# Kernel optimization log

Hardware: AMD Instinct MI355X
Metric: run time of the kernel (lower is better)

## Reference

```python
import jax, jax.numpy as jnp
import numpy as np

B, N = 16, 1023            # batch, signal length
T = N + 1                  # frames: hop=1, gaussian centers 0..N
F_BINS = N + 1             # rfft(2N) -> N+1 frequency bins
HID, NCLS = 128, 10


def setup_inputs() -> dict:
    key = jax.random.key(0)
    k = jax.random.split(key, 3)
    x = jax.random.normal(k[0], (B, N), dtype=jnp.float32)
    lambd = jnp.asarray(32.0, dtype=jnp.float32)  # learnable window width (sigma)
    feat = F_BINS * T
    W1 = jax.random.normal(k[1], (HID, feat), dtype=jnp.float32) / np.float32(np.sqrt(feat))
    b1 = jnp.zeros((HID,), jnp.float32)
    W2 = jax.random.normal(k[2], (NCLS, HID), dtype=jnp.float32) / np.float32(np.sqrt(HID))
    b2 = jnp.zeros((NCLS,), jnp.float32)
    return {"x": x, "lambd": lambd, "W1": W1, "b1": b1, "W2": W2, "b2": b2}


def _spectrogram(x, lambd):
    """Whole-signal differentiable Gaussian spectrogram (non-optimized path, hop=1).

    S[b, f, t] = | sum_n (x[b,n]-mean) * exp(-0.5*((n-t)/|lambd|)^2) * e^{-2pi i f n / (2N)} |^2
    Vectorized over the batch (replaces the per-sample Python loop).
    """
    n = x.shape[-1]
    sigma = jnp.abs(lambd)
    t = jnp.arange(n, dtype=jnp.float32)
    tc = jnp.arange(n + 1, dtype=jnp.float32)  # frame centers 0..n (n//hop + 1 frames)
    win = jnp.exp(-0.5 * ((t[None, :] - tc[:, None]) / sigma) ** 2)  # [T, n]
    xc = x - jnp.mean(x, axis=-1, keepdims=True)                     # per-sample mean removal
    xw = xc[:, None, :] * win[None]                                  # [B, T, n]
    spec = jnp.abs(jnp.fft.rfft(xw, n=2 * n, axis=-1)) ** 2          # [B, T, n+1]
    return jnp.transpose(spec, (0, 2, 1))[:, None]                   # [B, 1, n+1, T]


def reference(x, lambd, W1, b1, W2, b2):
    s = _spectrogram(x, lambd)                       # [B, 1, F_BINS, T]
    flat = s.reshape(s.shape[0], -1)                 # [B, F_BINS*T]
    h = jax.nn.relu(flat @ W1.T + b1)                # fc1 + relu
    out = h @ W2.T + b2                              # fc2
    return out, s
```

## Files before the change

### kernel.cpp

```cpp
#include <hip/hip_runtime.h>
#include <math.h>

#define NSIG   1023
#define BATCH  16
#define FT     1024
#define KW     256
#define RHALF  128
#define XPAD   1280
#define HID    128

#define OFF_XCP  0u
#define OFF_G    20480u
#define OFF_HRAW 20736u
#define OFF_TAB  22784u
#define TAB_ECH  0u
#define TAB_ECL  262144u
#define TAB_ESH  524288u
#define TAB_ESL  786432u

typedef int    i32x4  __attribute__((ext_vector_type(4)));
typedef float  f32x4  __attribute__((ext_vector_type(4)));
typedef __bf16 bf16x8 __attribute__((ext_vector_type(8)));
typedef unsigned short u16;

static __device__ __forceinline__ unsigned bfbits(float v) {
    unsigned u = __builtin_bit_cast(unsigned, v);
    return (u + 0x7fffu + ((u >> 16) & 1u)) >> 16;
}

__global__ void k_prep(const float* __restrict__ x, float* __restrict__ ws) {
    int b = blockIdx.x;
    __shared__ float red[256];
    float s = 0.f;
    for (int i = threadIdx.x; i < NSIG; i += 256) s += x[b * NSIG + i];
    red[threadIdx.x] = s;
    __syncthreads();
    for (int o = 128; o > 0; o >>= 1) {
        if (threadIdx.x < o) red[threadIdx.x] += red[threadIdx.x + o];
        __syncthreads();
    }
    float mean = red[0] * (1.0f / NSIG);
    float* xcp = ws + OFF_XCP + b * XPAD;
    for (int i = threadIdx.x; i < XPAD; i += 256) {
        int n = i - RHALF;
        xcp[i] = (n >= 0 && n < NSIG) ? (x[b * NSIG + n] - mean) : 0.f;
    }
}

__global__ void k_tables(const float* __restrict__ lambd, float* __restrict__ ws) {
    int bid = blockIdx.x;
    if (bid == 1024) {
        float sigma = fabsf(lambd[0]);
        float inv2s2 = 0.5f / (sigma * sigma);
        for (int i = threadIdx.x; i < KW; i += 256) {
            float d = (float)(i - RHALF);
            ws[OFF_G + i] = expf(-d * d * inv2s2);
        }
        for (int i = threadIdx.x; i < 2048; i += 256) ws[OFF_HRAW + i] = 0.f;
        return;
    }
    int idx = bid * 256 + threadIdx.x;
    int f = idx >> 8, k = idx & 255;
    int d = k - RHALF;
    int p = f * d;
    int m = p % 2046; if (m < 0) m += 2046;
    double ang = (double)m * (6.283185307179586476925286766559 / 2046.0);
    double sv, cv;
    sincos(ang, &sv, &cv);
    float cf = (float)cv, sf = (float)sv;
    u16* tab = (u16*)(ws + OFF_TAB);
    unsigned chb = bfbits(cf);
    float chf = __builtin_bit_cast(float, chb << 16);
    unsigned clb = bfbits(cf - chf);
    unsigned shb = bfbits(sf);
    float shf = __builtin_bit_cast(float, shb << 16);
    unsigned slb = bfbits(sf - shf);
    tab[TAB_ECH + idx] = (u16)chb;
    tab[TAB_ECL + idx] = (u16)clb;
    tab[TAB_ESH + idx] = (u16)shb;
    tab[TAB_ESL + idx] = (u16)slb;
}

__global__ __launch_bounds__(512, 4) void k_spec(const float* __restrict__ ws,
                                                 float* __restrict__ out) {
    __shared__ u16 yH[64 * 256];
    __shared__ u16 yL[64 * 256];
    int t0 = blockIdx.x * 64, f0 = blockIdx.y * 128, b = blockIdx.z;
    int tid = threadIdx.x;
    int wave = tid >> 6, lane = tid & 63;
    int lo = lane & 15, hi4 = lane >> 4;
    const u16* tab = (const u16*)(ws + OFF_TAB);
    const float* xcp = ws + OFF_XCP + b * XPAD;
    const float* gw  = ws + OFF_G;

    #pragma unroll
    for (int i = 0; i < 4; i++) {
        int idx = tid + i * 512;
        int t = idx >> 5, kg = idx & 31;
        int k = kg * 8;
        const float* xp = xcp + t0 + t + k;
        float4 g0 = *(const float4*)&gw[k];
        float4 g1 = *(const float4*)&gw[k + 4];
        float yv[8];
        yv[0] = xp[0] * g0.x; yv[1] = xp[1] * g0.y;
        yv[2] = xp[2] * g0.z; yv[3] = xp[3] * g0.w;
        yv[4] = xp[4] * g1.x; yv[5] = xp[5] * g1.y;
        yv[6] = xp[6] * g1.z; yv[7] = xp[7] * g1.w;
        unsigned hb[8], lb[8];
        #pragma unroll
        for (int j = 0; j < 8; j++) {
            unsigned u = __builtin_bit_cast(unsigned, yv[j]);
            unsigned h = (u + 0x7fffu + ((u >> 16) & 1u)) & 0xffff0000u;
            float hf = __builtin_bit_cast(float, h);
            hb[j] = h >> 16;
            lb[j] = bfbits(yv[j] - hf);
        }
        i32x4 ph, pl;
        ph.x = (int)(hb[0] | (hb[1] << 16)); ph.y = (int)(hb[2] | (hb[3] << 16));
        ph.z = (int)(hb[4] | (hb[5] << 16)); ph.w = (int)(hb[6] | (hb[7] << 16));
        pl.x = (int)(lb[0] | (lb[1] << 16)); pl.y = (int)(lb[2] | (lb[3] << 16));
        pl.z = (int)(lb[4] | (lb[5] << 16)); pl.w = (int)(lb[6] | (lb[7] << 16));
        int wb = ((t * 512 + kg * 16) ^ ((t & 7) << 4));
        *(i32x4*)((char*)yH + wb) = ph;
        *(i32x4*)((char*)yL + wb) = pl;
    }
    __syncthreads();

    size_t arow = (size_t)(f0 + wave * 16 + lo) * 256 + hi4 * 8;
    const u16* pech = tab + TAB_ECH + arow;
    const u16* pecl = tab + TAB_ECL + arow;
    const u16* pesh = tab + TAB_ESH + arow;
    const u16* pesl = tab + TAB_ESL + arow;

    f32x4 reA[4], imA[4];
    #pragma unroll
    for (int i = 0; i < 4; i++) {
        reA[i] = (f32x4){0.f, 0.f, 0.f, 0.f};
        imA[i] = (f32x4){0.f, 0.f, 0.f, 0.f};
    }

    #pragma unroll 2
    for (int c = 0; c < 8; c++) {
        i32x4 ech = *(const i32x4*)(pech + c * 32);
        i32x4 ecl = *(const i32x4*)(pecl + c * 32);
        i32x4 esh = *(const i32x4*)(pesh + c * 32);
        i32x4 esl = *(const i32x4*)(pesl + c * 32);
        #pragma unroll
        for (int tt = 0; tt < 4; tt++) {
            int tr = tt * 16 + lo;
            int rb = ((tr * 512 + c * 64 + hi4 * 16) ^ ((tr & 7) << 4));
            i32x4 yh = *(const i32x4*)((const char*)yH + rb);
            i32x4 yl = *(const i32x4*)((const char*)yL + rb);
            asm("v_mfma_f32_16x16x32_bf16 %0, %1, %2, %0" : "+v"(reA[tt]) : "v"(ech), "v"(yh));
            asm("v_mfma_f32_16x16x32_bf16 %0, %1, %2, %0" : "+v"(imA[tt]) : "v"(esh), "v"(yh));
            asm("v_mfma_f32_16x16x32_bf16 %0, %1, %2, %0" : "+v"(reA[tt]) : "v"(ech), "v"(yl));
            asm("v_mfma_f32_16x16x32_bf16 %0, %1, %2, %0" : "+v"(imA[tt]) : "v"(esh), "v"(yl));
            asm("v_mfma_f32_16x16x32_bf16 %0, %1, %2, %0" : "+v"(reA[tt]) : "v"(ecl), "v"(yh));
            asm("v_mfma_f32_16x16x32_bf16 %0, %1, %2, %0" : "+v"(imA[tt]) : "v"(esl), "v"(yh));
        }
    }
    asm volatile("s_nop 7\n\ts_nop 7");

    float* dS = out + 160;
    #pragma unroll
    for (int tt = 0; tt < 4; tt++) {
        #pragma unroll
        for (int r = 0; r < 4; r++) {
            int f = f0 + wave * 16 + hi4 * 4 + r;
            float re = reA[tt][r], im = imA[tt][r];
            dS[((size_t)b << 20) + (size_t)f * 1024 + t0 + tt * 16 + lo] = re * re + im * im;
        }
    }
}

static __device__ __forceinline__ bf16x8 packc4(float4 a, float4 b) {
    bf16x8 r;
    r[0] = (__bf16)a.x; r[1] = (__bf16)a.y; r[2] = (__bf16)a.z; r[3] = (__bf16)a.w;
    r[4] = (__bf16)b.x; r[5] = (__bf16)b.y; r[6] = (__bf16)b.z; r[7] = (__bf16)b.w;
    return r;
}
static __device__ __forceinline__ bf16x8 packcv(f32x4 a, f32x4 b) {
    bf16x8 r;
    r[0] = (__bf16)a.x; r[1] = (__bf16)a.y; r[2] = (__bf16)a.z; r[3] = (__bf16)a.w;
    r[4] = (__bf16)b.x; r[5] = (__bf16)b.y; r[6] = (__bf16)b.z; r[7] = (__bf16)b.w;
    return r;
}

static __device__ __forceinline__ void stageW(const float* base, float* dst,
                                              int rowLane, int colb0) {
    #pragma unroll
    for (int i = 0; i < 8; i++) {
        int sw = ((2 * (i & 3)) + rowLane) << 4;
        const float* src = base + (size_t)(2 * i + rowLane) * (1u << 20)
                         + ((colb0 ^ sw) >> 2);
        __builtin_amdgcn_global_load_lds(
            (const __attribute__((address_space(1))) void*)src,
            (__attribute__((address_space(3))) void*)((char*)dst + i * 1024),
            16, 0, 0);
    }
}

__global__ __launch_bounds__(256, 2) void k_fc1(const float* __restrict__ S,
                                                const float* __restrict__ W1,
                                                float* __restrict__ hraw) {
    __shared__ float Wl[4][2][2048];
    int tid = threadIdx.x;
    int wave = tid >> 6, lane = tid & 63;
    int jtg = blockIdx.x & 7;
    int ksg = blockIdx.x >> 3;
    int ks  = (ksg << 2) | wave;
    int bq = lane >> 4, lo = lane & 15;
    int rowLane = lane >> 5;
    int colb0 = (lane & 31) << 4;
    int sw = (lo & 7) << 4;

    const float* Sp = S + (size_t)lo * (1u << 20) + (size_t)ks * 512 + bq * 8;
    const float* Wb = W1 + (size_t)(jtg * 16) * (1u << 20) + (size_t)ks * 512;
    float* buf0 = &Wl[wave][0][0];
    float* buf1 = &Wl[wave][1][0];

    f32x4 acc = {0.f, 0.f, 0.f, 0.f};

    stageW(Wb, buf0, rowLane, colb0);

    #pragma unroll
    for (int s = 0; s < 4; s++) {
        float4 sA0[4], sA1[4];
        #pragma unroll
        for (int c = 0; c < 4; c++) {
            const float* sp = Sp + s * 128 + c * 32;
            sA0[c] = *(const float4*)(sp);
            sA1[c] = *(const float4*)(sp + 4);
        }
        if (s < 3) {
            stageW(Wb + (s + 1) * 128, (s & 1) ? buf0 : buf1, rowLane, colb0);
            asm volatile("s_waitcnt vmcnt(8)" ::: "memory");
        } else {
            asm volatile("s_waitcnt vmcnt(0)" ::: "memory");
        }
        const char* wb = (const char*)((s & 1) ? buf1 : buf0);
        #pragma unroll
        for (int c = 0; c < 4; c++) {
            f32x4 w0 = *(const f32x4*)(wb + lo * 512 + ((c * 128 + bq * 32) ^ sw));
            f32x4 w1 = *(const f32x4*)(wb + lo * 512 + ((c * 128 + bq * 32 + 16) ^ sw));
            acc = __builtin_amdgcn_mfma_f32_16x16x32_bf16(packc4(sA0[c], sA1[c]),
                                                          packcv(w0, w1), acc, 0, 0, 0);
        }
    }

    float* red = &Wl[wave][0][0];
    #pragma unroll
    for (int r = 0; r < 4; r++) red[(bq * 4 + r) * 16 + lo] = acc[r];
    __syncthreads();
    float v = Wl[0][0][tid & 255] + Wl[1][0][tid & 255]
            + Wl[2][0][tid & 255] + Wl[3][0][tid & 255];
    atomicAdd(&hraw[(tid >> 4) * HID + jtg * 16 + (tid & 15)], v);
}

__global__ void k_head(const float* __restrict__ hraw, const float* __restrict__ b1,
                       const float* __restrict__ W2, const float* __restrict__ b2,
                       float* __restrict__ out) {
    __shared__ float hl[2048];
    int tid = threadIdx.x;
    for (int p = tid; p < 2048; p += 256) {
        float hv = hraw[p] + b1[p & 127];
        hl[p] = hv > 0.f ? hv : 0.f;
    }
    __syncthreads();
    if (tid < 160) {
        int b = tid / 10, c = tid - b * 10;
        float s = b2[c];
        for (int j = 0; j < 128; j++) s += hl[b * 128 + j] * W2[c * 128 + j];
        out[b * 10 + c] = s;
    }
}

extern "C" void kernel_launch(void* const* d_in, const int* in_sizes, int n_in,
                              void* d_out, int out_size, void* d_ws, size_t ws_size,
                              hipStream_t stream) {
    const float* x     = (const float*)d_in[0];
    const float* lambd = (const float*)d_in[1];
    const float* W1    = (const float*)d_in[2];
    const float* b1    = (const float*)d_in[3];
    const float* W2    = (const float*)d_in[4];
    const float* b2    = (const float*)d_in[5];
    float* out = (float*)d_out;
    float* ws  = (float*)d_ws;

    hipLaunchKernelGGL(k_prep,   dim3(16),         dim3(256), 0, stream, x, ws);
    hipLaunchKernelGGL(k_tables, dim3(1025),       dim3(256), 0, stream, lambd, ws);
    hipLaunchKernelGGL(k_spec,   dim3(16, 8, 16),  dim3(512), 0, stream, ws, out);
    hipLaunchKernelGGL(k_fc1,    dim3(4096),       dim3(256), 0, stream,
                       out + 160, W1, ws + OFF_HRAW);
    hipLaunchKernelGGL(k_head,   dim3(1),          dim3(256), 0, stream,
                       ws + OFF_HRAW, b1, W2, b2, out);
}
```

Before: 238.3 us.

## Reuse spectrogram A-fragments across all eight fc1 output tiles per block

Each fc1 block now handles every one of the 128 hidden units (eight 16-column tiles) for its K slice instead of one tile. The S activations are loaded and packed to bf16 once per K step and reused for eight MFMA tiles. This cuts redundant S reads eightfold and reduces the grid from 4096 to 512 blocks. The trade-offs are more accumulator registers, fewer blocks to hide W1 streaming latency, and more atomics per block at the end.

New measurement: 202.4 us. 15.1% less time.

```diff
diff --git a/kernel.cpp b/kernel.cpp
--- a/kernel.cpp
+++ b/kernel.cpp
@@ -206,55 +206,92 @@
     __shared__ float Wl[4][2][2048];
     int tid = threadIdx.x;
     int wave = tid >> 6, lane = tid & 63;
-    int jtg = blockIdx.x & 7;
-    int ksg = blockIdx.x >> 3;
-    int ks  = (ksg << 2) | wave;
     int bq = lane >> 4, lo = lane & 15;
+    int ks = (blockIdx.x << 2) | wave;
+    size_t kb = (size_t)ks * 512;
+
     int rowLane = lane >> 5;
     int colb0 = (lane & 31) << 4;
     int sw = (lo & 7) << 4;
 
-    const float* Sp = S + (size_t)lo * (1u << 20) + (size_t)ks * 512 + bq * 8;
-    const float* Wb = W1 + (size_t)(jtg * 16) * (1u << 20) + (size_t)ks * 512;
+    const float* Sp = S + ((size_t)lo << 20) + kb + bq * 8;
     float* buf0 = &Wl[wave][0][0];
     float* buf1 = &Wl[wave][1][0];
 
-    f32x4 acc = {0.f, 0.f, 0.f, 0.f};
-
-    stageW(Wb, buf0, rowLane, colb0);
-
-    #pragma unroll
-    for (int s = 0; s < 4; s++) {
-        float4 sA0[4], sA1[4];
-        #pragma unroll
-        for (int c = 0; c < 4; c++) {
-            const float* sp = Sp + s * 128 + c * 32;
-            sA0[c] = *(const float4*)(sp);
-            sA1[c] = *(const float4*)(sp + 4);
-        }
-        if (s < 3) {
-            stageW(Wb + (s + 1) * 128, (s & 1) ? buf0 : buf1, rowLane, colb0);
+    f32x4 acc[8];
+    #pragma unroll
+    for (int j = 0; j < 8; j++) acc[j] = (f32x4){0.f, 0.f, 0.f, 0.f};
+
+    stageW(W1 + kb, buf0, rowLane, colb0);
+
+    bf16x8 af0, af1, af2, af3;
+
+    #pragma unroll
+    for (int c = 0; c < 32; c++) {
+        const int s = c >> 3, jt = c & 7;
+        float4 sA[8];
+        if (jt == 0) {
+            const float* sp = Sp + s * 128;
+            #pragma unroll
+            for (int q = 0; q < 4; q++) {
+                sA[2 * q]     = *(const float4*)(sp + q * 32);
+                sA[2 * q + 1] = *(const float4*)(sp + q * 32 + 4);
+            }
+        }
+        if (c < 31) {
+            const int cn = c + 1, sn = cn >> 3, jn = cn & 7;
+            stageW(W1 + ((size_t)(jn * 16) << 20) + kb + sn * 128,
+                   (c & 1) ? buf0 : buf1, rowLane, colb0);
             asm volatile("s_waitcnt vmcnt(8)" ::: "memory");
         } else {
             asm volatile("s_waitcnt vmcnt(0)" ::: "memory");
         }
-        const char* wb = (const char*)((s & 1) ? buf1 : buf0);
+        if (jt == 0) {
+            af0 = packc4(sA[0], sA[1]);
+            af1 = packc4(sA[2], sA[3]);
+            af2 = packc4(sA[4], sA[5]);
+            af3 = packc4(sA[6], sA[7]);
+        }
+        const char* wb = (const char*)((c & 1) ? buf1 : buf0);
+        {
+            int cb = 0 * 128 + bq * 32;
+            f32x4 w0 = *(const f32x4*)(wb + lo * 512 + (cb ^ sw));
+            f32x4 w1 = *(const f32x4*)(wb + lo * 512 + ((cb + 16) ^ sw));
+            acc[jt] = __builtin_amdgcn_mfma_f32_16x16x32_bf16(af0, packcv(w0, w1), acc[jt], 0, 0, 0);
+        }
+        {
+            int cb = 1 * 128 + bq * 32;
+            f32x4 w0 = *(const f32x4*)(wb + lo * 512 + (cb ^ sw));
+            f32x4 w1 = *(const f32x4*)(wb + lo * 512 + ((cb + 16) ^ sw));
+            acc[jt] = __builtin_amdgcn_mfma_f32_16x16x32_bf16(af1, packcv(w0, w1), acc[jt], 0, 0, 0);
+        }
+        {
+            int cb = 2 * 128 + bq * 32;
+            f32x4 w0 = *(const f32x4*)(wb + lo * 512 + (cb ^ sw));
+            f32x4 w1 = *(const f32x4*)(wb + lo * 512 + ((cb + 16) ^ sw));
+            acc[jt] = __builtin_amdgcn_mfma_f32_16x16x32_bf16(af2, packcv(w0, w1), acc[jt], 0, 0, 0);
+        }
+        {
+            int cb = 3 * 128 + bq * 32;
+            f32x4 w0 = *(const f32x4*)(wb + lo * 512 + (cb ^ sw));
+            f32x4 w1 = *(const f32x4*)(wb + lo * 512 + ((cb + 16) ^ sw));
+            acc[jt] = __builtin_amdgcn_mfma_f32_16x16x32_bf16(af3, packcv(w0, w1), acc[jt], 0, 0, 0);
+        }
+    }
+
+    float* red = &Wl[wave][0][0];
+    #pragma unroll
+    for (int jt = 0; jt < 8; jt++) {
         #pragma unroll
-        for (int c = 0; c < 4; c++) {
-            f32x4 w0 = *(const f32x4*)(wb + lo * 512 + ((c * 128 + bq * 32) ^ sw));
-            f32x4 w1 = *(const f32x4*)(wb + lo * 512 + ((c * 128 + bq * 32 + 16) ^ sw));
-            acc = __builtin_amdgcn_mfma_f32_16x16x32_bf16(packc4(sA0[c], sA1[c]),
-                                                          packcv(w0, w1), acc, 0, 0, 0);
-        }
-    }
-
-    float* red = &Wl[wave][0][0];
-    #pragma unroll
-    for (int r = 0; r < 4; r++) red[(bq * 4 + r) * 16 + lo] = acc[r];
+        for (int r = 0; r < 4; r++) {
+            red[(bq * 4 + r) * 128 + jt * 16 + lo] = acc[jt][r];
+        }
+    }
     __syncthreads();
-    float v = Wl[0][0][tid & 255] + Wl[1][0][tid & 255]
-            + Wl[2][0][tid & 255] + Wl[3][0][tid & 255];
-    atomicAdd(&hraw[(tid >> 4) * HID + jtg * 16 + (tid & 15)], v);
+    for (int p = tid; p < 2048; p += 256) {
+        float v = Wl[0][0][p] + Wl[1][0][p] + Wl[2][0][p] + Wl[3][0][p];
+        atomicAdd(&hraw[p], v);
+    }
 }
 
 __global__ void k_head(const float* __restrict__ hraw, const float* __restrict__ b1,
@@ -290,7 +327,7 @@
     hipLaunchKernelGGL(k_prep,   dim3(16),         dim3(256), 0, stream, x, ws);
     hipLaunchKernelGGL(k_tables, dim3(1025),       dim3(256), 0, stream, lambd, ws);
     hipLaunchKernelGGL(k_spec,   dim3(16, 8, 16),  dim3(512), 0, stream, ws, out);
-    hipLaunchKernelGGL(k_fc1,    dim3(4096),       dim3(256), 0, stream,
+    hipLaunchKernelGGL(k_fc1,    dim3(512),        dim3(256), 0, stream,
                        out + 160, W1, ws + OFF_HRAW);
     hipLaunchKernelGGL(k_head,   dim3(1),          dim3(256), 0, stream,
                        ws + OFF_HRAW, b1, W2, b2, out);
```
